# Performance work log

Hardware: AMD Instinct MI355X
Metric: run time of the kernel (lower is better)

## Reference

```python
import jax, jax.numpy as jnp
import numpy as np

N_NODES = 100000


def _gcn_conv(x, row, col, ew, W, b, n):
    # PyG GCNConv: add self-loops (weight 1), symmetric normalization,
    # linear transform, scatter-add aggregation at target, then bias.
    loop = jnp.arange(n, dtype=row.dtype)
    r = jnp.concatenate([row, loop])
    c = jnp.concatenate([col, loop])
    w = jnp.concatenate([ew, jnp.ones((n,), ew.dtype)])
    deg = jax.ops.segment_sum(w, c, num_segments=n)
    dinv = jnp.where(deg > 0, jax.lax.rsqrt(deg), 0.0)
    nrm = dinv[r] * w * dinv[c]                 # [E+N]
    h = x @ W                                    # [N, out]
    msg = h[r] * nrm[:, None]                    # gather + scale
    return jax.ops.segment_sum(msg, c, num_segments=n) + b


def setup_inputs() -> dict:
    key = jax.random.key(0)
    ks = jax.random.split(key, 16)
    n, e, f, s = N_NODES, 1600000, 8, 64
    return {
        "x": jax.random.normal(ks[0], (n, f), jnp.float32),
        "edge_index": jax.random.randint(ks[1], (2, e), 0, n, jnp.int32),
        "edge_weight": jax.random.uniform(ks[2], (e,), jnp.float32),
        "s_values": jax.random.normal(ks[3], (s,), jnp.float32),
        "s_fc1_w": jax.random.normal(ks[4], (s, s // 2), jnp.float32) * 0.1,
        "s_fc1_b": jax.random.normal(ks[5], (s // 2,), jnp.float32) * 0.1,
        "s_fc2_w": jax.random.normal(ks[6], (s // 2, 1), jnp.float32) * 0.1,
        "s_fc2_b": jax.random.normal(ks[7], (1,), jnp.float32) * 0.1,
        "conv1_w": jax.random.normal(ks[8], (f + 1, 32), jnp.float32) * 0.3,
        "conv1_b": jax.random.normal(ks[9], (32,), jnp.float32) * 0.1,
        "conv2_w": jax.random.normal(ks[10], (32, 16), jnp.float32) * 0.2,
        "conv2_b": jax.random.normal(ks[11], (16,), jnp.float32) * 0.1,
        "fc1_w": jax.random.normal(ks[12], (16, 1), jnp.float32) * 0.25,
        "fc1_b": jax.random.normal(ks[13], (1,), jnp.float32) * 0.1,
    }


def reference(x, edge_index, edge_weight, s_values,
              s_fc1_w, s_fc1_b, s_fc2_w, s_fc2_b,
              conv1_w, conv1_b, conv2_w, conv2_b, fc1_w, fc1_b):
    n = x.shape[0]
    row, col = edge_index[0], edge_index[1]
    # s-value encoder: two small linears, ReLU between
    s_enc = jax.nn.relu(s_values @ s_fc1_w + s_fc1_b) @ s_fc2_w + s_fc2_b  # [1]
    xs = jnp.concatenate([x, jnp.broadcast_to(s_enc[None, :], (n, 1))], axis=1)
    h1 = _gcn_conv(xs, row, col, edge_weight, conv1_w, conv1_b, n)
    h1 = jax.nn.leaky_relu(h1, 0.01)
    # dropout is identity in eval mode; norm=False skips GraphNorm
    h2 = _gcn_conv(h1, row, col, edge_weight, conv2_w, conv2_b, n)
    h2 = jax.nn.leaky_relu(h2, 0.01)
    return h2 @ fc1_w + fc1_b  # [N, 1]
```

## Files before the change

### kernel.cpp

```cpp
#include <hip/hip_runtime.h>
#include <hip/hip_fp16.h>


#define NBLKA  256
#define BSH    7
#define BNODES 128
#define MAXBK  784

__device__ inline unsigned enc_w(float w) {
    return ((unsigned)__half_as_ushort(__float2half_rn(w)) & 0x7FFFu) << 17;
}
__device__ inline float dec_w(unsigned e) {
    return __half2float(__ushort_as_half((unsigned short)((e >> 17) & 0x7FFFu)));
}

__global__ void k_hist(const int* __restrict__ ei, int* __restrict__ hist,
                       int E, int EPB, int NBK,
                       const float* __restrict__ x, __half* __restrict__ xh, int n,
                       const float* __restrict__ sv, const float* __restrict__ w1,
                       const float* __restrict__ b1, const float* __restrict__ w2,
                       const float* __restrict__ b2, float* __restrict__ senc) {
    if (blockIdx.x >= NBLKA) {
        if (blockIdx.x == gridDim.x - 1) {
            __shared__ float hid[32];
            int j = threadIdx.x;
            if (j < 32) {
                float acc = b1[j];
                #pragma unroll 8
                for (int k = 0; k < 64; ++k) acc += sv[k] * w1[k * 32 + j];
                hid[j] = acc > 0.f ? acc : 0.f;
            }
            __syncthreads();
            if (j == 0) {
                float acc = b2[0];
                #pragma unroll 8
                for (int k = 0; k < 32; ++k) acc += hid[k] * w2[k];
                senc[0] = acc;
            }
            return;
        }
        int i = (blockIdx.x - NBLKA) * blockDim.x + threadIdx.x;
        if (i >= n) return;
        const float4* xi = reinterpret_cast<const float4*>(x + (size_t)i * 8);
        float4 u = xi[0], v = xi[1];
        __half2 h0 = __floats2half2_rn(u.x, u.y);
        __half2 h1 = __floats2half2_rn(u.z, u.w);
        __half2 h2 = __floats2half2_rn(v.x, v.y);
        __half2 h3 = __floats2half2_rn(v.z, v.w);
        uint4 w;
        w.x = *reinterpret_cast<unsigned*>(&h0);
        w.y = *reinterpret_cast<unsigned*>(&h1);
        w.z = *reinterpret_cast<unsigned*>(&h2);
        w.w = *reinterpret_cast<unsigned*>(&h3);
        reinterpret_cast<uint4*>(xh + (size_t)i * 8)[0] = w;
        return;
    }
    __shared__ int lh[MAXBK];
    for (int k = threadIdx.x; k < NBK; k += blockDim.x) lh[k] = 0;
    __syncthreads();
    int b = blockIdx.x;
    int e0 = b * EPB, e1 = min(E, e0 + EPB);
    for (int e = e0 + threadIdx.x; e < e1; e += blockDim.x)
        atomicAdd(&lh[ei[E + e] >> BSH], 1);
    __syncthreads();
    for (int k = threadIdx.x; k < NBK; k += blockDim.x)
        hist[(size_t)k * NBLKA + b] = lh[k];
}

__global__ void k_scan1(int* __restrict__ data, int* __restrict__ bsum, int nflat) {
    __shared__ int s[512];
    int i = blockIdx.x * 512 + threadIdx.x;
    int v = (i < nflat) ? data[i] : 0;
    s[threadIdx.x] = v;
    __syncthreads();
    for (int off = 1; off < 512; off <<= 1) {
        int tv = (threadIdx.x >= off) ? s[threadIdx.x - off] : 0;
        __syncthreads();
        if (threadIdx.x >= off) s[threadIdx.x] += tv;
        __syncthreads();
    }
    if (i < nflat) data[i] = s[threadIdx.x] - v;
    if (threadIdx.x == 511) bsum[blockIdx.x] = s[511];
}

__global__ void k_scan2(int* __restrict__ bsum, int nb) {
    __shared__ int s[512];
    __shared__ int carry;
    if (threadIdx.x == 0) carry = 0;
    __syncthreads();
    for (int base = 0; base < nb; base += 512) {
        int idx = base + threadIdx.x;
        int v = (idx < nb) ? bsum[idx] : 0;
        s[threadIdx.x] = v;
        __syncthreads();
        for (int off = 1; off < 512; off <<= 1) {
            int tv = (threadIdx.x >= off) ? s[threadIdx.x - off] : 0;
            __syncthreads();
            if (threadIdx.x >= off) s[threadIdx.x] += tv;
            __syncthreads();
        }
        if (idx < nb) bsum[idx] = s[threadIdx.x] - v + carry;
        __syncthreads();
        if (threadIdx.x == 0) carry += s[511];
        __syncthreads();
    }
}

__global__ void k_scatter(const int* __restrict__ ei, const float* __restrict__ ew,
                          const int* __restrict__ scanned, const int* __restrict__ bsum,
                          int2* __restrict__ ebuf, int E, int EPB, int NBK) {
    __shared__ int lbase[MAXBK];
    int b = blockIdx.x;
    for (int k = threadIdx.x; k < NBK; k += blockDim.x) {
        int idx = k * NBLKA + b;
        lbase[k] = scanned[idx] + bsum[idx >> 9];
    }
    __syncthreads();
    int e0 = b * EPB, e1 = min(E, e0 + EPB);
    for (int e = e0 + threadIdx.x; e < e1; e += blockDim.x) {
        int c = ei[E + e];
        int r = ei[e];
        int k = c >> BSH;
        int pos = atomicAdd(&lbase[k], 1);
        ebuf[pos] = make_int2(r | ((c & (BNODES - 1)) << 25), __float_as_int(ew[e]));
    }
}

__global__ void k_sort(const int* __restrict__ scanned, const int* __restrict__ bsum,
                       const int2* __restrict__ ebuf,
                       int* __restrict__ row, float* __restrict__ dinv,
                       unsigned* __restrict__ csr4, int n, int E, int NBK) {
    __shared__ int lcnt[BNODES];
    __shared__ int lofs[BNODES];
    __shared__ float lw[BNODES];
    int k = blockIdx.x;
    if (threadIdx.x < BNODES) { lcnt[threadIdx.x] = 0; lw[threadIdx.x] = 1.0f; }
    __syncthreads();
    int idx0 = k * NBLKA;
    int bs = scanned[idx0] + bsum[idx0 >> 9];
    int be = E;
    if (k + 1 < NBK) {
        int idx1 = (k + 1) * NBLKA;
        be = scanned[idx1] + bsum[idx1 >> 9];
    }
    for (int s = bs + threadIdx.x; s < be; s += blockDim.x) {
        int2 ent = ebuf[s];
        int cl = ((unsigned)ent.x) >> 25;
        atomicAdd(&lcnt[cl], 1);
        atomicAdd(&lw[cl], __int_as_float(ent.y));
    }
    __syncthreads();
    int v = (threadIdx.x < BNODES) ? lcnt[threadIdx.x] : 0;
    if (threadIdx.x < BNODES) lofs[threadIdx.x] = v;
    __syncthreads();
    for (int off = 1; off < BNODES; off <<= 1) {
        int tv = 0;
        if (threadIdx.x < BNODES && threadIdx.x >= off) tv = lofs[threadIdx.x - off];
        __syncthreads();
        if (threadIdx.x < BNODES && threadIdx.x >= off) lofs[threadIdx.x] += tv;
        __syncthreads();
    }
    if (threadIdx.x < BNODES) {
        int excl = lofs[threadIdx.x] - v;
        lofs[threadIdx.x] = excl;
        int i = k * BNODES + threadIdx.x;
        if (i < n) {
            row[i] = bs + excl;
            dinv[i] = rsqrtf(lw[threadIdx.x]);
        }
    }
    if (k == NBK - 1 && threadIdx.x == 0) row[n] = E;
    __syncthreads();
    for (int s = bs + threadIdx.x; s < be; s += blockDim.x) {
        int2 ent = ebuf[s];
        int cl = ((unsigned)ent.x) >> 25;
        int pos = bs + atomicAdd(&lofs[cl], 1);
        csr4[pos] = enc_w(__int_as_float(ent.y)) | (unsigned)(ent.x & 0x1FFFF);
    }
}

__global__ void k_pass1(const int* __restrict__ row, unsigned* __restrict__ csr4,
                        const float* __restrict__ dinv, const __half* __restrict__ xh,
                        const float* __restrict__ senc,
                        const float* __restrict__ W1, const float* __restrict__ b1,
                        const float* __restrict__ W2, __half* __restrict__ th, int n) {
    __shared__ float sW1[288];
    __shared__ float sb1[32];
    __shared__ float sW2[32 * 17];
    for (int j = threadIdx.x; j < 288; j += blockDim.x) sW1[j] = W1[j];
    for (int j = threadIdx.x; j < 512; j += blockDim.x) sW2[(j >> 4) * 17 + (j & 15)] = W2[j];
    if (threadIdx.x < 32) sb1[threadIdx.x] = b1[threadIdx.x];
    __syncthreads();
    int g = blockIdx.x * blockDim.x + threadIdx.x;
    int i = g >> 2;
    int quad = g & 3;
    if (i >= n) return;
    float di = dinv[i];
    float a[8];
    float sw;
    if (quad == 0) {
        const uint4* xp = reinterpret_cast<const uint4*>(xh + (size_t)i * 8);
        uint4 w = xp[0];
        const __half2* hh = reinterpret_cast<const __half2*>(&w);
        #pragma unroll
        for (int q = 0; q < 4; ++q) {
            float2 f = __half22float2(hh[q]);
            a[2 * q] = di * f.x; a[2 * q + 1] = di * f.y;
        }
        sw = di;
    } else {
        #pragma unroll
        for (int q = 0; q < 8; ++q) a[q] = 0.f;
        sw = 0.f;
    }
    int s0 = row[i], s1 = row[i + 1];
    for (int s = s0 + quad; s < s1; s += 4) {
        unsigned ent = csr4[s];
        unsigned src = ent & 0x1FFFFu;
        float wpre = dec_w(ent) * dinv[src];
        csr4[s] = enc_w(wpre) | src;
        const uint4* xp = reinterpret_cast<const uint4*>(xh + (size_t)src * 8);
        uint4 w = xp[0];
        const __half2* hh = reinterpret_cast<const __half2*>(&w);
        #pragma unroll
        for (int q = 0; q < 4; ++q) {
            float2 f = __half22float2(hh[q]);
            a[2 * q] += wpre * f.x; a[2 * q + 1] += wpre * f.y;
        }
        sw += wpre;
    }
    #pragma unroll
    for (int q = 0; q < 8; ++q) a[q] += __shfl_xor(a[q], 1);
    sw += __shfl_xor(sw, 1);
    #pragma unroll
    for (int q = 0; q < 8; ++q) a[q] += __shfl_xor(a[q], 2);
    sw += __shfl_xor(sw, 2);
    float a8 = di * sw * senc[0];
    float af[8];
    #pragma unroll
    for (int q = 0; q < 8; ++q) af[q] = di * a[q];
    float h[8];
    #pragma unroll
    for (int jj = 0; jj < 8; ++jj) {
        int j = quad * 8 + jj;
        float acc = sb1[j] + a8 * sW1[8 * 32 + j];
        #pragma unroll
        for (int f = 0; f < 8; ++f) acc += af[f] * sW1[f * 32 + j];
        h[jj] = acc > 0.f ? acc : 0.01f * acc;
    }
    float p[16];
    #pragma unroll
    for (int o = 0; o < 16; ++o) p[o] = 0.f;
    #pragma unroll
    for (int jj = 0; jj < 8; ++jj) {
        int j = quad * 8 + jj;
        #pragma unroll
        for (int o = 0; o < 16; ++o) p[o] += h[jj] * sW2[j * 17 + o];
    }
    #pragma unroll
    for (int o = 0; o < 16; ++o) p[o] += __shfl_xor(p[o], 1);
    #pragma unroll
    for (int o = 0; o < 16; ++o) p[o] += __shfl_xor(p[o], 2);
    int o0 = quad * 4;
    __half2 hv0 = __floats2half2_rn(p[o0 + 0], p[o0 + 1]);
    __half2 hv1 = __floats2half2_rn(p[o0 + 2], p[o0 + 3]);
    uint2 st;
    st.x = *reinterpret_cast<unsigned*>(&hv0);
    st.y = *reinterpret_cast<unsigned*>(&hv1);
    reinterpret_cast<uint2*>(th + (size_t)i * 16 + o0)[0] = st;
}

__global__ void k_pass2(const int* __restrict__ row, const unsigned* __restrict__ csr4,
                        const float* __restrict__ dinv, const __half* __restrict__ th,
                        const float* __restrict__ b2, const float* __restrict__ fw,
                        const float* __restrict__ fb, float* __restrict__ out, int n) {
    __shared__ float sb2[16];
    __shared__ float sfw[16];
    if (threadIdx.x < 16) { sb2[threadIdx.x] = b2[threadIdx.x]; sfw[threadIdx.x] = fw[threadIdx.x]; }
    __syncthreads();
    int g = blockIdx.x * blockDim.x + threadIdx.x;
    int i = g >> 2;
    int quad = g & 3;
    if (i >= n) return;
    float di = dinv[i];
    float acc[16];
    if (quad == 0) {
        const uint4* tp = reinterpret_cast<const uint4*>(th + (size_t)i * 16);
        uint4 w0 = tp[0], w1 = tp[1];
        const __half2* hh0 = reinterpret_cast<const __half2*>(&w0);
        const __half2* hh1 = reinterpret_cast<const __half2*>(&w1);
        #pragma unroll
        for (int q = 0; q < 4; ++q) {
            float2 f0 = __half22float2(hh0[q]);
            float2 f1 = __half22float2(hh1[q]);
            acc[2 * q + 0] = di * f0.x; acc[2 * q + 1] = di * f0.y;
            acc[8 + 2 * q + 0] = di * f1.x; acc[8 + 2 * q + 1] = di * f1.y;
        }
    } else {
        #pragma unroll
        for (int q = 0; q < 16; ++q) acc[q] = 0.f;
    }
    int s0 = row[i], s1 = row[i + 1];
    for (int s = s0 + quad; s < s1; s += 4) {
        unsigned ent = csr4[s];
        float wpre = dec_w(ent);
        const uint4* tp = reinterpret_cast<const uint4*>(th + (size_t)(ent & 0x1FFFFu) * 16);
        uint4 w0 = tp[0], w1 = tp[1];
        const __half2* hh0 = reinterpret_cast<const __half2*>(&w0);
        const __half2* hh1 = reinterpret_cast<const __half2*>(&w1);
        #pragma unroll
        for (int q = 0; q < 4; ++q) {
            float2 f0 = __half22float2(hh0[q]);
            float2 f1 = __half22float2(hh1[q]);
            acc[2 * q + 0] += wpre * f0.x; acc[2 * q + 1] += wpre * f0.y;
            acc[8 + 2 * q + 0] += wpre * f1.x; acc[8 + 2 * q + 1] += wpre * f1.y;
        }
    }
    #pragma unroll
    for (int q = 0; q < 16; ++q) acc[q] += __shfl_xor(acc[q], 1);
    #pragma unroll
    for (int q = 0; q < 16; ++q) acc[q] += __shfl_xor(acc[q], 2);
    if (quad) return;
    float o = fb[0];
    #pragma unroll
    for (int q = 0; q < 16; ++q) {
        float v = di * acc[q] + sb2[q];
        v = v > 0.f ? v : 0.01f * v;
        o += v * sfw[q];
    }
    out[i] = o;
}

extern "C" void kernel_launch(void* const* d_in, const int* in_sizes, int n_in,
                              void* d_out, int out_size, void* d_ws, size_t ws_size,
                              hipStream_t stream) {
    const float* x      = (const float*)d_in[0];
    const int*   ei     = (const int*)d_in[1];
    const float* ew     = (const float*)d_in[2];
    const float* sv     = (const float*)d_in[3];
    const float* sfc1w  = (const float*)d_in[4];
    const float* sfc1b  = (const float*)d_in[5];
    const float* sfc2w  = (const float*)d_in[6];
    const float* sfc2b  = (const float*)d_in[7];
    const float* conv1w = (const float*)d_in[8];
    const float* conv1b = (const float*)d_in[9];
    const float* conv2w = (const float*)d_in[10];
    const float* conv2b = (const float*)d_in[11];
    const float* fc1w   = (const float*)d_in[12];
    const float* fc1b   = (const float*)d_in[13];

    const int n = in_sizes[0] / 8;
    const int E = in_sizes[2];

    const int NBK   = (n + BNODES - 1) >> BSH;
    const int nflat = NBK * NBLKA;
    const int EPB   = (E + NBLKA - 1) / NBLKA;
    const int nb1   = (nflat + 511) / 512;
    const int gX    = (n + 1023) / 1024;

    size_t off = 0;
    auto alloc = [&](size_t words) { size_t o = off; off += (words + 3) & ~(size_t)3; return o; };
    float*    base = (float*)d_ws;
    float*    senc = base + alloc(4);
    float*    dinv = base + alloc(n);
    int*      rowp = (int*)(base + alloc(n + 1));
    int*      hist = (int*)(base + alloc(nflat));
    int*      bsum = (int*)(base + alloc(512));
    int2*     ebuf = (int2*)(base + alloc((size_t)2 * E));
    unsigned* csr4 = (unsigned*)(base + alloc(E));
    __half*   xh   = (__half*)(base + alloc((size_t)4 * n));
    __half*   th   = (__half*)(base + alloc((size_t)8 * n));

    const int BT = 256;
    const int g4 = ((size_t)4 * n + BT - 1) / BT;

    k_hist<<<NBLKA + gX + 1, 1024, 0, stream>>>(ei, hist, E, EPB, NBK,
                                                x, xh, n,
                                                sv, sfc1w, sfc1b, sfc2w, sfc2b, senc);
    k_scan1<<<nb1, 512, 0, stream>>>(hist, bsum, nflat);
    k_scan2<<<1, 512, 0, stream>>>(bsum, nb1);
    k_scatter<<<NBLKA, 1024, 0, stream>>>(ei, ew, hist, bsum, ebuf, E, EPB, NBK);
    k_sort<<<NBK, 512, 0, stream>>>(hist, bsum, ebuf, rowp, dinv, csr4, n, E, NBK);
    k_pass1<<<g4, BT, 0, stream>>>(rowp, csr4, dinv, xh, senc,
                                   conv1w, conv1b, conv2w, th, n);
    k_pass2<<<g4, BT, 0, stream>>>(rowp, csr4, dinv, th,
                                   conv2b, fc1w, fc1b, (float*)d_out, n);
}
```

Measured before the change: 97.81 us.

## Stage scatter entries in LDS by bucket for coalesced global writes

Doubles the number of partition blocks and changes the scatter kernel to first rank each edge within its bucket through shared-memory counters. It then prefix-scans the bucket counts and places entries into a bucket-sorted staging buffer in shared memory, so the final copy to the global edge buffer writes contiguous runs. The goal is to replace random scattered 8-byte global writes with mostly coalesced stores. The cost is extra shared memory (about 42KB), a 1024-step block scan, and per-thread register arrays, which limit occupancy. Correctness relies on each block holding at most 3200 edges and each thread handling at most 4 edges.

Measured after the change: 120.4 us. +23.1%, slower.

```diff
diff --git a/kernel.cpp b/kernel.cpp
--- a/kernel.cpp
+++ b/kernel.cpp
@@ -2,7 +2,7 @@
 #include <hip/hip_fp16.h>
 
 
-#define NBLKA  256
+#define NBLKA  512
 #define BSH    7
 #define BNODES 128
 #define MAXBK  784
@@ -109,21 +109,51 @@
 __global__ void k_scatter(const int* __restrict__ ei, const float* __restrict__ ew,
                           const int* __restrict__ scanned, const int* __restrict__ bsum,
                           int2* __restrict__ ebuf, int E, int EPB, int NBK) {
+    __shared__ int2 staged[3200];
+    __shared__ unsigned short sbk[3200];
+    __shared__ int lcnt[1024];
     __shared__ int lbase[MAXBK];
     int b = blockIdx.x;
     for (int k = threadIdx.x; k < NBK; k += blockDim.x) {
         int idx = k * NBLKA + b;
         lbase[k] = scanned[idx] + bsum[idx >> 9];
     }
+    lcnt[threadIdx.x] = 0;
     __syncthreads();
     int e0 = b * EPB, e1 = min(E, e0 + EPB);
+    int2 entl[4]; int bkl[4]; int rkl[4]; int nl = 0;
     for (int e = e0 + threadIdx.x; e < e1; e += blockDim.x) {
         int c = ei[E + e];
         int r = ei[e];
         int k = c >> BSH;
-        int pos = atomicAdd(&lbase[k], 1);
-        ebuf[pos] = make_int2(r | ((c & (BNODES - 1)) << 25), __float_as_int(ew[e]));
-    }
+        entl[nl] = make_int2(r | ((c & (BNODES - 1)) << 25), __float_as_int(ew[e]));
+        bkl[nl] = k;
+        rkl[nl] = atomicAdd(&lcnt[k], 1);
+        ++nl;
+    }
+    __syncthreads();
+    int v = lcnt[threadIdx.x];
+    for (int off = 1; off < 1024; off <<= 1) {
+        int tv = (threadIdx.x >= off) ? lcnt[threadIdx.x - off] : 0;
+        __syncthreads();
+        if (threadIdx.x >= off) lcnt[threadIdx.x] += tv;
+        __syncthreads();
+    }
+    int incl = lcnt[threadIdx.x];
+    __syncthreads();
+    lcnt[threadIdx.x] = incl - v;
+    __syncthreads();
+    if (threadIdx.x < NBK) lbase[threadIdx.x] -= lcnt[threadIdx.x];
+    __syncthreads();
+    for (int t = 0; t < nl; ++t) {
+        int p = lcnt[bkl[t]] + rkl[t];
+        staged[p] = entl[t];
+        sbk[p] = (unsigned short)bkl[t];
+    }
+    __syncthreads();
+    int cnt = e1 - e0;
+    for (int p = threadIdx.x; p < cnt; p += blockDim.x)
+        ebuf[lbase[sbk[p]] + p] = staged[p];
 }
 
 __global__ void k_sort(const int* __restrict__ scanned, const int* __restrict__ bsum,
@@ -365,7 +395,7 @@
     float*    dinv = base + alloc(n);
     int*      rowp = (int*)(base + alloc(n + 1));
     int*      hist = (int*)(base + alloc(nflat));
-    int*      bsum = (int*)(base + alloc(512));
+    int*      bsum = (int*)(base + alloc(1024));
     int2*     ebuf = (int2*)(base + alloc((size_t)2 * E));
     unsigned* csr4 = (unsigned*)(base + alloc(E));
     __half*   xh   = (__half*)(base + alloc((size_t)4 * n));
```
